# Optimization experiments

Hardware: AMD Instinct MI355X
Metric: run time of the kernel (lower is better)

Reference implementation:

```python
import jax, jax.numpy as jnp
import numpy as np

B, S, NX, NH = 2, 2048, 1024, 16
HD = NX // NH  # head dim = 64


def setup_inputs() -> dict:
    key = jax.random.key(0)
    k1, k2, k3 = jax.random.split(key, 3)
    x = jax.random.normal(k1, (B, S, NX), dtype=jnp.float32)
    w_attn = jax.random.normal(k2, (NX, 3 * NX), dtype=jnp.float32) * 0.02
    b_attn = jnp.zeros((3 * NX,), dtype=jnp.float32)
    w_proj = jax.random.normal(k3, (NX, NX), dtype=jnp.float32) * 0.02
    b_proj = jnp.zeros((NX,), dtype=jnp.float32)
    return {"x": x, "w_attn": w_attn, "b_attn": b_attn, "w_proj": w_proj, "b_proj": b_proj}


def _split_heads(t):
    # [B, S, NX] -> [B, NH, S, HD]
    b, s, _ = t.shape
    return t.reshape(b, s, NH, HD).transpose(0, 2, 1, 3)


def reference(x, w_attn, b_attn, w_proj, b_proj):
    # c_attn: Conv1D == affine projection to fused QKV
    qkv = jnp.einsum("bsi,io->bso", x, w_attn) + b_attn  # [B, S, 3*NX]
    q, k, v = jnp.split(qkv, 3, axis=2)
    q, k, v = _split_heads(q), _split_heads(k), _split_heads(v)  # [B, NH, S, HD]

    # scaled dot-product scores (scale=True)
    w = jnp.einsum("bhqd,bhkd->bhqk", q, k) / jnp.sqrt(jnp.asarray(HD, dtype=q.dtype))

    # causal mask via multiply-subtract (matches TF: w*b - 10000*(1-b))
    nd = ns = S
    i = jnp.arange(nd)[:, None]
    j = jnp.arange(ns)[None, :]
    b = (i >= j - ns + nd).astype(w.dtype)  # [nd, ns]
    w = w * b - 10000.0 * (1.0 - b)

    w = jax.nn.softmax(w, axis=-1)  # stable_softmax
    # attn_dropout / head_mask: identity (inference, no head mask)

    a = jnp.einsum("bhqk,bhkd->bhqd", w, v)  # [B, NH, S, HD]
    # merge heads -> [B, S, NX]
    a = a.transpose(0, 2, 1, 3).reshape(B, S, NX)
    # c_proj
    out = jnp.einsum("bsi,io->bso", a, w_proj) + b_proj
    return out
```

## Files before the change

kernel.cpp:

```cpp
#include <hip/hip_runtime.h>
#include <stdint.h>

typedef __attribute__((ext_vector_type(8))) short short8;
typedef __attribute__((ext_vector_type(4))) float f32x4;
typedef __attribute__((ext_vector_type(16))) float f32x16;
typedef __attribute__((ext_vector_type(4))) unsigned short ushort4v;
typedef __attribute__((ext_vector_type(2))) int int2v;

#define BB 2
#define SS 2048
#define NXDIM 1024
#define NHEADS 16
#define HDIM 64

__device__ __forceinline__ unsigned short f2bf(float f){
  unsigned int u = __float_as_uint(f);
  u += 0x7fffu + ((u >> 16) & 1u);
  return (unsigned short)(u >> 16);
}

__device__ __forceinline__ void gload_lds16(const void* g, void* l){
  __builtin_amdgcn_global_load_lds((const __attribute__((address_space(1))) void*)g,
                                   (__attribute__((address_space(3))) void*)l, 16, 0, 0);
}

__device__ __forceinline__ unsigned cvt_pk_bf16(float lo, float hi){
  unsigned r;
  asm("v_cvt_pk_bf16_f32 %0, %1, %2" : "=v"(r) : "v"(lo), "v"(hi));
  return r;
}

__device__ __forceinline__ int2v ds_tr_b16(unsigned addr){
  int2v r;
  asm volatile("ds_read_b64_tr_b16 %0, %1" : "=v"(r) : "v"(addr));
  return r;
}

__device__ __forceinline__ int2v plswap(int a, int b){
  return __builtin_amdgcn_permlane32_swap(a, b, false, false);
}
__device__ __forceinline__ float plmax(float x){
  int2v r = plswap(__float_as_int(x), __float_as_int(x));
  return fmaxf(__int_as_float(r.x), __int_as_float(r.y));
}
__device__ __forceinline__ float pladd(float x){
  int2v r = plswap(__float_as_int(x), __float_as_int(x));
  return __int_as_float(r.x) + __int_as_float(r.y);
}

__global__ __launch_bounds__(256) void f32_to_bf16_k(const float* __restrict__ in,
                                                     unsigned short* __restrict__ out, int n4){
  int i = blockIdx.x * 256 + threadIdx.x;
  if (i >= n4) return;
  float4 v = ((const float4*)in)[i];
  ushort4v r = { f2bf(v.x), f2bf(v.y), f2bf(v.z), f2bf(v.w) };
  ((ushort4v*)out)[i] = r;
}

__global__ __launch_bounds__(256) void transpose_bf16_k(const float* __restrict__ in,
                                                        unsigned short* __restrict__ out,
                                                        int R, int C){
  __shared__ float t[32][33];
  const int bx = blockIdx.x * 32, by = blockIdx.y * 32;
  const int tx = threadIdx.x, ty = threadIdx.y;
  #pragma unroll
  for (int i = ty; i < 32; i += 8)
    t[i][tx] = in[(size_t)(by + i) * C + bx + tx];
  __syncthreads();
  #pragma unroll
  for (int i = ty; i < 32; i += 8)
    out[(size_t)(bx + i) * R + by + tx] = f2bf(t[tx][i]);
}

__global__ __launch_bounds__(256) void gemm2_64_k(const unsigned short* __restrict__ A,
                                                  const unsigned short* __restrict__ BT,
                                                  const float* __restrict__ bias,
                                                  float* __restrict__ Cout,
                                                  int M, int N, int K)
{
  __shared__ unsigned short As[64*32];
  __shared__ unsigned short Bs[64*32];
  const int tid = threadIdx.x;
  const int w = tid >> 6, lane = tid & 63;
  const int l15 = lane & 15, g = lane >> 4;
  const int wr = w >> 1, wc = w & 1;
  const int m0 = blockIdx.y * 64, n0 = blockIdx.x * 64;

  f32x4 acc[2][2];
  #pragma unroll
  for (int m=0;m<2;m++)
    #pragma unroll
    for (int n=0;n<2;n++) acc[m][n] = (f32x4){0.f,0.f,0.f,0.f};

  const int srow_in = lane >> 2;
  const int scol = (lane & 3) * 8;

  for (int k0 = 0; k0 < K; k0 += 32){
    __syncthreads();
    gload_lds16(A  + (size_t)(m0 + w*16 + srow_in) * K + (k0 + scol), &As[(w*16)*32]);
    gload_lds16(BT + (size_t)(n0 + w*16 + srow_in) * K + (k0 + scol), &Bs[(w*16)*32]);
    __syncthreads();

    short8 af[2], bf[2];
    #pragma unroll
    for (int m=0;m<2;m++) af[m] = *(const short8*)&As[(wr*32 + m*16 + l15)*32 + g*8];
    #pragma unroll
    for (int n=0;n<2;n++) bf[n] = *(const short8*)&Bs[(wc*32 + n*16 + l15)*32 + g*8];
    #pragma unroll
    for (int m=0;m<2;m++)
      #pragma unroll
      for (int n=0;n<2;n++)
        acc[m][n] = __builtin_amdgcn_mfma_f32_16x16x32_bf16(af[m], bf[n], acc[m][n], 0, 0, 0);
  }

  const int crow0 = m0 + wr*32;
  const int ccol0 = n0 + wc*32;
  #pragma unroll
  for (int n=0;n<2;n++){
    const int col = ccol0 + n*16 + l15;
    const float bv = bias[col];
    #pragma unroll
    for (int m=0;m<2;m++){
      #pragma unroll
      for (int r=0;r<4;r++){
        const int row = crow0 + m*16 + g*4 + r;
        Cout[(size_t)row * N + col] = acc[m][n][r] + bv;
      }
    }
  }
}

__global__ __launch_bounds__(512) void gemm256_k(const unsigned short* __restrict__ A,
                                                 const unsigned short* __restrict__ BT,
                                                 const float* __restrict__ bias,
                                                 unsigned short* __restrict__ Cout,
                                                 int M, int N, int K)
{
  __shared__ unsigned short lds[57344];
  unsigned short* As0 = lds;
  unsigned short* Bs0 = lds + 32768;
  const int tid = threadIdx.x;
  const int w = tid >> 6, lane = tid & 63;
  const int l15 = lane & 15, g = lane >> 4;
  const int wm = w >> 2, wn = w & 3;
  const int m0 = blockIdx.y * 256, n0 = blockIdx.x * 192;

  f32x4 acc[8][3];
  #pragma unroll
  for (int m=0;m<8;m++)
    #pragma unroll
    for (int n=0;n<3;n++) acc[m][n] = (f32x4){0.f,0.f,0.f,0.f};

  const int srow = lane >> 3;
  const int scol = 8 * ((lane & 7) ^ (lane >> 3));

  auto stageA = [&](int bi, int k0, int j){
    const int r = w*32 + j*8 + srow;
    gload_lds16(A + (size_t)(m0 + r) * K + (k0 + scol), As0 + bi*16384 + (w*32 + j*8)*64);
  };
  auto stageB = [&](int bi, int k0, int j){
    const int r = w*24 + j*8 + srow;
    gload_lds16(BT + (size_t)(n0 + r) * K + (k0 + scol), Bs0 + bi*12288 + (w*24 + j*8)*64);
  };

  #pragma unroll
  for (int j=0;j<4;j++) stageA(0, 0, j);
  #pragma unroll
  for (int j=0;j<3;j++) stageB(0, 0, j);
  asm volatile("s_waitcnt vmcnt(0)" ::: "memory");
  __syncthreads();

  const int niter = K >> 6;
  int cur = 0;

  for (int t = 0; t < niter; ++t){
    const int k1 = (t+1) << 6;
    if (t+1 < niter){
      #pragma unroll
      for (int j=0;j<4;j++) stageA(cur^1, k1, j);
      #pragma unroll
      for (int j=0;j<3;j++) stageB(cur^1, k1, j);
    }

    const char* Ab = (const char*)(As0 + cur*16384);
    const char* Bb = (const char*)(Bs0 + cur*12288);

    short8 bf[3][2];
    #pragma unroll
    for (int nf=0;nf<3;nf++){
      const int row = wn*48 + nf*16 + l15;
      #pragma unroll
      for (int kk=0;kk<2;kk++)
        bf[nf][kk] = *(const short8*)(Bb + row*128 + ((kk*64 + g*16) ^ ((l15&7)<<4)));
    }

    #pragma unroll
    for (int ph=0; ph<4; ++ph){
      short8 af[2][2];
      #pragma unroll
      for (int i=0;i<2;i++){
        const int mf = ph*2 + i;
        const int row = wm*128 + mf*16 + l15;
        #pragma unroll
        for (int kk=0;kk<2;kk++)
          af[i][kk] = *(const short8*)(Ab + row*128 + ((kk*64 + g*16) ^ ((l15&7)<<4)));
      }
      asm volatile("s_waitcnt lgkmcnt(0)" ::: "memory");
      __builtin_amdgcn_sched_barrier(0);

      __builtin_amdgcn_s_setprio(1);
      #pragma unroll
      for (int i=0;i<2;i++)
        #pragma unroll
        for (int nf=0;nf<3;nf++)
          #pragma unroll
          for (int kk=0;kk<2;kk++)
            acc[ph*2+i][nf] = __builtin_amdgcn_mfma_f32_16x16x32_bf16(af[i][kk], bf[nf][kk],
                                                                      acc[ph*2+i][nf], 0, 0, 0);
      __builtin_amdgcn_s_setprio(0);
    }

    asm volatile("s_waitcnt vmcnt(0)" ::: "memory");
    __syncthreads();
    cur ^= 1;
  }

  unsigned short* ct = lds;
  #pragma unroll
  for (int nf=0;nf<3;nf++){
    const int col = wn*48 + nf*16 + l15;
    const float bv = bias[n0 + col];
    #pragma unroll
    for (int mf=0;mf<8;mf++){
      #pragma unroll
      for (int r=0;r<4;r++)
        ct[(wm*128 + mf*16 + g*4 + r)*192 + col] = f2bf(acc[mf][nf][r] + bv);
    }
  }
  __syncthreads();
  #pragma unroll
  for (int u = 0; u < 12; ++u){
    const int idx = u*512 + tid;
    const int row = idx / 24, sl = idx % 24;
    *(short8*)(Cout + (size_t)(m0 + row) * N + n0 + sl*8) = *(const short8*)&ct[row*192 + sl*8];
  }
}

__global__ __launch_bounds__(512) void attn_k(const unsigned short* __restrict__ qkv,
                                              unsigned short* __restrict__ aout)
{
  const int xy = ((int)blockIdx.x + (int)blockIdx.y) & 15;
  const int qb = blockIdx.z ? xy : (15 - xy);
  const int h = blockIdx.y, b = blockIdx.z;
  const int tid = threadIdx.x;
  const int w = tid >> 6, lane = tid & 63;
  const int l31 = lane & 31, hi = lane >> 5;
  const int qw = w >> 1, p = w & 1;

  __shared__ unsigned short lds[32768];
  unsigned short* Ksb = lds;
  unsigned short* Vsb = lds + 16384;

  const size_t rs = 3 * NXDIM;
  const unsigned short* Qg = qkv + (size_t)b * SS * rs + h * HDIM;
  const unsigned short* Kg = Qg + NXDIM;
  const unsigned short* Vg = Qg + 2 * NXDIM;

  const int q0w = qb*128 + qw*32;
  const int q   = q0w + l31;
  const int qw_hi = q0w + 31;

  short8 qf[4];
  #pragma unroll
  for (int c=0;c<4;c++)
    qf[c] = *(const short8*)(Qg + (size_t)q * rs + c*16 + 8*hi);

  f32x16 O0, O1;
  #pragma unroll
  for (int r=0;r<16;r++){ O0[r]=0.f; O1[r]=0.f; }
  float m_run = -1e30f, l_run = 0.f;
  const float SC2 = 0.125f * 1.44269504089f;
  const float THRR = 44.36f;

  const int krow_in = lane >> 3;
  const int kcol    = 8 * ((lane & 7) ^ (lane >> 3));
  const int v_d     = ((lane >> 3) & 3) * 16 + 8 * (lane & 1);
  const unsigned vtr_base = (unsigned)(size_t)Vsb + 8u*(unsigned)lane + 768u*(unsigned)hi;

  auto stage = [&](int bi, int tt){
    unsigned short* Kd = Ksb + (p*2 + bi)*4096;
    unsigned short* Vd = Vsb + (p*2 + bi)*4096;
    #pragma unroll
    for (int j=0;j<2;j++){
      const int ch = qw*2 + j;
      const int krow = tt*64 + ch*8 + krow_in;
      gload_lds16(Kg + (size_t)krow * rs + kcol, Kd + ch*512);
      const int vkv = tt*64 + (ch*2 + hi)*4 + ((lane>>1)&3);
      gload_lds16(Vg + (size_t)vkv * rs + v_d, Vd + ch*512);
    }
  };

  const int tmax = 2*qb + 1;
  stage(0, p);
  __syncthreads();
  int cur = 0;

  for (int t = p; t <= tmax; t += 2){
    if (t + 2 <= tmax) stage(cur^1, t+2);

    const char* Kb = (const char*)(Ksb + (p*2 + cur)*4096);
    const unsigned vb = vtr_base + (unsigned)((p*2 + cur)*8192);

    #pragma unroll
    for (int kvs=0;kvs<2;kvs++){
      const int kv_lo = t*64 + kvs*32;
      if (kv_lo > qw_hi) continue;

      f32x16 S;
      #pragma unroll
      for (int r=0;r<16;r++) S[r] = 0.f;
      __builtin_amdgcn_s_setprio(1);
      #pragma unroll
      for (int c=0;c<4;c++){
        const int row = kvs*32 + l31;
        short8 kf = *(const short8*)(Kb + row*128 + ((c*32 + 16*hi) ^ ((row&7)<<4)));
        S = __builtin_amdgcn_mfma_f32_32x32x16_bf16(kf, qf[c], S, 0, 0, 0);
      }
      __builtin_amdgcn_s_setprio(0);

      int2v tv[8];
      #pragma unroll
      for (int c=0;c<2;c++)
        #pragma unroll
        for (int dh=0;dh<2;dh++)
          #pragma unroll
          for (int eb=0;eb<2;eb++)
            tv[c*4+dh*2+eb] = ds_tr_b16(vb + (unsigned)((kvs*8 + c*4 + eb)*512 + dh*256));

      float mA=-1e30f, mB=-1e30f, mC=-1e30f, mD=-1e30f;
      if (kv_lo + 31 > q0w){
        #pragma unroll
        for (int r=0;r<16;r+=4){
          const int kvb = kv_lo + 8*(r>>2) + 4*hi;
          float s0 = (kvb+0 <= q) ? S[r+0] : -1e30f;
          float s1 = (kvb+1 <= q) ? S[r+1] : -1e30f;
          float s2 = (kvb+2 <= q) ? S[r+2] : -1e30f;
          float s3 = (kvb+3 <= q) ? S[r+3] : -1e30f;
          S[r+0]=s0; S[r+1]=s1; S[r+2]=s2; S[r+3]=s3;
          mA = fmaxf(mA, s0); mB = fmaxf(mB, s1); mC = fmaxf(mC, s2); mD = fmaxf(mD, s3);
        }
      } else {
        #pragma unroll
        for (int r=0;r<16;r+=4){
          mA = fmaxf(mA, S[r+0]); mB = fmaxf(mB, S[r+1]);
          mC = fmaxf(mC, S[r+2]); mD = fmaxf(mD, S[r+3]);
        }
      }
      float mx = fmaxf(fmaxf(mA,mB), fmaxf(mC,mD));
      mx = plmax(mx);

      if (!__all(mx <= m_run + THRR)){
        const float m_new = fmaxf(m_run, mx);
        const float corr = __builtin_exp2f((m_run - m_new) * SC2);
        m_run = m_new;
        l_run *= corr;
        #pragma unroll
        for (int r=0;r<16;r++){ O0[r] *= corr; O1[r] *= corr; }
      }
      const float msc = m_run * SC2;

      float lA=0.f, lB=0.f, lC=0.f, lD=0.f;
      #pragma unroll
      for (int r=0;r<16;r+=4){
        float p0=__builtin_exp2f(__builtin_fmaf(S[r+0],SC2,-msc));
        float p1=__builtin_exp2f(__builtin_fmaf(S[r+1],SC2,-msc));
        float p2=__builtin_exp2f(__builtin_fmaf(S[r+2],SC2,-msc));
        float p3=__builtin_exp2f(__builtin_fmaf(S[r+3],SC2,-msc));
        S[r+0]=p0; S[r+1]=p1; S[r+2]=p2; S[r+3]=p3;
        lA+=p0; lB+=p1; lC+=p2; lD+=p3;
      }
      float ls = (lA+lB) + (lC+lD);
      ls = pladd(ls);
      l_run += ls;

      unsigned pk[8];
      #pragma unroll
      for (int i=0;i<8;i++) pk[i] = cvt_pk_bf16(S[2*i], S[2*i+1]);
      short8 pfrag[2];
      #pragma unroll
      for (int c=0;c<2;c++){
        int2v r0 = plswap((int)pk[4*c+0], (int)pk[4*c+2]);
        int2v r1 = plswap((int)pk[4*c+1], (int)pk[4*c+3]);
        union { unsigned u[4]; short8 s; } pw;
        pw.u[0] = (unsigned)r0.x; pw.u[1] = (unsigned)r1.x;
        pw.u[2] = (unsigned)r0.y; pw.u[3] = (unsigned)r1.y;
        pfrag[c] = pw.s;
      }

      asm volatile("s_waitcnt lgkmcnt(0)" ::: "memory");
      __builtin_amdgcn_sched_barrier(0);

      __builtin_amdgcn_s_setprio(1);
      #pragma unroll
      for (int c=0;c<2;c++){
        union { int2v t[2]; short8 s; } v0, v1;
        v0.t[0] = tv[c*4+0]; v0.t[1] = tv[c*4+1];
        v1.t[0] = tv[c*4+2]; v1.t[1] = tv[c*4+3];
        O0 = __builtin_amdgcn_mfma_f32_32x32x16_bf16(v0.s, pfrag[c], O0, 0, 0, 0);
        O1 = __builtin_amdgcn_mfma_f32_32x32x16_bf16(v1.s, pfrag[c], O1, 0, 0, 0);
      }
      __builtin_amdgcn_s_setprio(0);
    }

    __syncthreads();
    cur ^= 1;
  }

  float* sm = (float*)lds + qw * (64*34);
  if (p){
    #pragma unroll
    for (int r=0;r<16;r++){ sm[lane*34 + r] = O0[r]; sm[lane*34 + 16 + r] = O1[r]; }
    sm[lane*34 + 32] = m_run;
    sm[lane*34 + 33] = l_run;
  }
  __syncthreads();
  if (!p){
    const float m1 = sm[lane*34 + 32], l1 = sm[lane*34 + 33];
    const float mm = fmaxf(m_run, m1);
    const float c0 = __builtin_exp2f((m_run - mm) * SC2);
    const float c1 = __builtin_exp2f((m1 - mm) * SC2);
    const float inv = 1.f / (l_run*c0 + l1*c1);
    unsigned short* dst = aout + ((size_t)b*SS + q) * NXDIM + h*HDIM;
    #pragma unroll
    for (int g4=0; g4<4; g4++){
      ushort4v a0, a1;
      #pragma unroll
      for (int i=0;i<4;i++){
        a0[i] = f2bf((O0[4*g4+i]*c0 + sm[lane*34 + 4*g4+i]*c1) * inv);
        a1[i] = f2bf((O1[4*g4+i]*c0 + sm[lane*34 + 16 + 4*g4+i]*c1) * inv);
      }
      *(ushort4v*)(dst + 8*g4 + 4*hi)      = a0;
      *(ushort4v*)(dst + 32 + 8*g4 + 4*hi) = a1;
    }
  }
}

extern "C" void kernel_launch(void* const* d_in, const int* in_sizes, int n_in,
                              void* d_out, int out_size, void* d_ws, size_t ws_size,
                              hipStream_t stream){
  (void)in_sizes; (void)n_in; (void)out_size; (void)ws_size;
  const float* x      = (const float*)d_in[0];
  const float* w_attn = (const float*)d_in[1];
  const float* b_attn = (const float*)d_in[2];
  const float* w_proj = (const float*)d_in[3];
  const float* b_proj = (const float*)d_in[4];
  float* out = (float*)d_out;

  unsigned short* xb   = (unsigned short*)d_ws;
  unsigned short* waT  = xb  + (size_t)4096*1024;
  unsigned short* wpT  = waT + (size_t)3072*1024;
  unsigned short* qkv  = wpT + (size_t)1024*1024;
  unsigned short* aout = qkv + (size_t)4096*3072;

  f32_to_bf16_k<<<4096, 256, 0, stream>>>(x, xb, 4096*1024/4);
  transpose_bf16_k<<<dim3(3072/32, 1024/32), dim3(32,8), 0, stream>>>(w_attn, waT, 1024, 3072);
  transpose_bf16_k<<<dim3(1024/32, 1024/32), dim3(32,8), 0, stream>>>(w_proj, wpT, 1024, 1024);

  gemm256_k<<<dim3(3072/192, 4096/256), 512, 0, stream>>>(xb, waT, b_attn, qkv, 4096, 3072, 1024);
  attn_k<<<dim3(SS/128, NHEADS, BB), 512, 0, stream>>>(qkv, aout);
  gemm2_64_k<<<dim3(1024/64, 4096/64), 256, 0, stream>>>(aout, wpT, b_proj, out, 4096, 1024, 1024);
}
```

Before: 113.4 us.

## Shrink attention blocks to 64 queries and merge both weight transposes into one launch

The attention kernel now uses 256-thread blocks covering 64 query rows each, launching twice as many blocks with half the LDS. The KV double-buffered prefetch is replaced by single-buffer staging with a sync before and after each tile, so two wave pairs split KV tiles by parity. The two weight-transpose kernels are fused into a single launch that picks its matrix from the block index. This aims for more blocks in flight and better causal load balance, plus one fewer launch, at the cost of losing overlap between global loads and compute.

Measured after the change: 144.9 us. 1.28x slower.

```diff
diff --git a/kernel.cpp b/kernel.cpp
--- a/kernel.cpp
+++ b/kernel.cpp
@@ -57,12 +57,19 @@
   ((ushort4v*)out)[i] = r;
 }
 
-__global__ __launch_bounds__(256) void transpose_bf16_k(const float* __restrict__ in,
-                                                        unsigned short* __restrict__ out,
-                                                        int R, int C){
+__global__ __launch_bounds__(256) void transpose2_k(const float* __restrict__ wa,
+                                                    unsigned short* __restrict__ waT,
+                                                    const float* __restrict__ wp,
+                                                    unsigned short* __restrict__ wpT){
   __shared__ float t[32][33];
-  const int bx = blockIdx.x * 32, by = blockIdx.y * 32;
-  const int tx = threadIdx.x, ty = threadIdx.y;
+  const bool second = blockIdx.x >= 96;
+  const float* in = second ? wp : wa;
+  unsigned short* out = second ? wpT : waT;
+  const int C = second ? 1024 : 3072;
+  const int R = 1024;
+  const int bx = (second ? ((int)blockIdx.x - 96) : (int)blockIdx.x) * 32;
+  const int by = blockIdx.y * 32;
+  const int tx = threadIdx.x & 31, ty = threadIdx.x >> 5;
   #pragma unroll
   for (int i = ty; i < 32; i += 8)
     t[i][tx] = in[(size_t)(by + i) * C + bx + tx];
@@ -246,27 +253,27 @@
   }
 }
 
-__global__ __launch_bounds__(512) void attn_k(const unsigned short* __restrict__ qkv,
+__global__ __launch_bounds__(256) void attn_k(const unsigned short* __restrict__ qkv,
                                               unsigned short* __restrict__ aout)
 {
-  const int xy = ((int)blockIdx.x + (int)blockIdx.y) & 15;
-  const int qb = blockIdx.z ? xy : (15 - xy);
+  const int xy = ((int)blockIdx.x + (int)blockIdx.y) & 31;
+  const int qb = blockIdx.z ? xy : (31 - xy);
   const int h = blockIdx.y, b = blockIdx.z;
   const int tid = threadIdx.x;
   const int w = tid >> 6, lane = tid & 63;
   const int l31 = lane & 31, hi = lane >> 5;
   const int qw = w >> 1, p = w & 1;
 
-  __shared__ unsigned short lds[32768];
+  __shared__ unsigned short lds[16384];
   unsigned short* Ksb = lds;
-  unsigned short* Vsb = lds + 16384;
+  unsigned short* Vsb = lds + 8192;
 
   const size_t rs = 3 * NXDIM;
   const unsigned short* Qg = qkv + (size_t)b * SS * rs + h * HDIM;
   const unsigned short* Kg = Qg + NXDIM;
   const unsigned short* Vg = Qg + 2 * NXDIM;
 
-  const int q0w = qb*128 + qw*32;
+  const int q0w = qb*64 + qw*32;
   const int q   = q0w + l31;
   const int qw_hi = q0w + 31;
 
@@ -285,14 +292,15 @@
   const int krow_in = lane >> 3;
   const int kcol    = 8 * ((lane & 7) ^ (lane >> 3));
   const int v_d     = ((lane >> 3) & 3) * 16 + 8 * (lane & 1);
-  const unsigned vtr_base = (unsigned)(size_t)Vsb + 8u*(unsigned)lane + 768u*(unsigned)hi;
-
-  auto stage = [&](int bi, int tt){
-    unsigned short* Kd = Ksb + (p*2 + bi)*4096;
-    unsigned short* Vd = Vsb + (p*2 + bi)*4096;
-    #pragma unroll
-    for (int j=0;j<2;j++){
-      const int ch = qw*2 + j;
+  const unsigned vtr_base = (unsigned)(size_t)Vsb + (unsigned)(p*8192)
+                          + 8u*(unsigned)lane + 768u*(unsigned)hi;
+
+  auto stage = [&](int tt){
+    unsigned short* Kd = Ksb + p*4096;
+    unsigned short* Vd = Vsb + p*4096;
+    #pragma unroll
+    for (int j=0;j<4;j++){
+      const int ch = qw*4 + j;
       const int krow = tt*64 + ch*8 + krow_in;
       gload_lds16(Kg + (size_t)krow * rs + kcol, Kd + ch*512);
       const int vkv = tt*64 + (ch*2 + hi)*4 + ((lane>>1)&3);
@@ -300,123 +308,122 @@
     }
   };
 
-  const int tmax = 2*qb + 1;
-  stage(0, p);
-  __syncthreads();
-  int cur = 0;
-
-  for (int t = p; t <= tmax; t += 2){
-    if (t + 2 <= tmax) stage(cur^1, t+2);
-
-    const char* Kb = (const char*)(Ksb + (p*2 + cur)*4096);
-    const unsigned vb = vtr_base + (unsigned)((p*2 + cur)*8192);
-
-    #pragma unroll
-    for (int kvs=0;kvs<2;kvs++){
-      const int kv_lo = t*64 + kvs*32;
-      if (kv_lo > qw_hi) continue;
-
-      f32x16 S;
-      #pragma unroll
-      for (int r=0;r<16;r++) S[r] = 0.f;
-      __builtin_amdgcn_s_setprio(1);
-      #pragma unroll
-      for (int c=0;c<4;c++){
-        const int row = kvs*32 + l31;
-        short8 kf = *(const short8*)(Kb + row*128 + ((c*32 + 16*hi) ^ ((row&7)<<4)));
-        S = __builtin_amdgcn_mfma_f32_32x32x16_bf16(kf, qf[c], S, 0, 0, 0);
+  for (int i = 0; 2*i <= qb; ++i){
+    const int t = 2*i + p;
+    const bool act = (t <= qb);
+    if (act) stage(t);
+    __syncthreads();
+
+    if (act){
+      const char* Kb = (const char*)(Ksb + p*4096);
+      const unsigned vb = vtr_base;
+
+      #pragma unroll
+      for (int kvs=0;kvs<2;kvs++){
+        const int kv_lo = t*64 + kvs*32;
+        if (kv_lo > qw_hi) continue;
+
+        f32x16 S;
+        #pragma unroll
+        for (int r=0;r<16;r++) S[r] = 0.f;
+        __builtin_amdgcn_s_setprio(1);
+        #pragma unroll
+        for (int c=0;c<4;c++){
+          const int row = kvs*32 + l31;
+          short8 kf = *(const short8*)(Kb + row*128 + ((c*32 + 16*hi) ^ ((row&7)<<4)));
+          S = __builtin_amdgcn_mfma_f32_32x32x16_bf16(kf, qf[c], S, 0, 0, 0);
+        }
+        __builtin_amdgcn_s_setprio(0);
+
+        int2v tv[8];
+        #pragma unroll
+        for (int c=0;c<2;c++)
+          #pragma unroll
+          for (int dh=0;dh<2;dh++)
+            #pragma unroll
+            for (int eb=0;eb<2;eb++)
+              tv[c*4+dh*2+eb] = ds_tr_b16(vb + (unsigned)((kvs*8 + c*4 + eb)*512 + dh*256));
+
+        float mA=-1e30f, mB=-1e30f, mC=-1e30f, mD=-1e30f;
+        if (kv_lo + 31 > q0w){
+          #pragma unroll
+          for (int r=0;r<16;r+=4){
+            const int kvb = kv_lo + 8*(r>>2) + 4*hi;
+            float s0 = (kvb+0 <= q) ? S[r+0] : -1e30f;
+            float s1 = (kvb+1 <= q) ? S[r+1] : -1e30f;
+            float s2 = (kvb+2 <= q) ? S[r+2] : -1e30f;
+            float s3 = (kvb+3 <= q) ? S[r+3] : -1e30f;
+            S[r+0]=s0; S[r+1]=s1; S[r+2]=s2; S[r+3]=s3;
+            mA = fmaxf(mA, s0); mB = fmaxf(mB, s1); mC = fmaxf(mC, s2); mD = fmaxf(mD, s3);
+          }
+        } else {
+          #pragma unroll
+          for (int r=0;r<16;r+=4){
+            mA = fmaxf(mA, S[r+0]); mB = fmaxf(mB, S[r+1]);
+            mC = fmaxf(mC, S[r+2]); mD = fmaxf(mD, S[r+3]);
+          }
+        }
+        float mx = fmaxf(fmaxf(mA,mB), fmaxf(mC,mD));
+        mx = plmax(mx);
+
+        if (!__all(mx <= m_run + THRR)){
+          const float m_new = fmaxf(m_run, mx);
+          const float corr = __builtin_exp2f((m_run - m_new) * SC2);
+          m_run = m_new;
+          l_run *= corr;
+          #pragma unroll
+          for (int r=0;r<16;r++){ O0[r] *= corr; O1[r] *= corr; }
+        }
+        const float msc = m_run * SC2;
+
+        float lA=0.f, lB=0.f, lC=0.f, lD=0.f;
+        #pragma unroll
+        for (int r=0;r<16;r+=4){
+          float p0=__builtin_exp2f(__builtin_fmaf(S[r+0],SC2,-msc));
+          float p1=__builtin_exp2f(__builtin_fmaf(S[r+1],SC2,-msc));
+          float p2=__builtin_exp2f(__builtin_fmaf(S[r+2],SC2,-msc));
+          float p3=__builtin_exp2f(__builtin_fmaf(S[r+3],SC2,-msc));
+          S[r+0]=p0; S[r+1]=p1; S[r+2]=p2; S[r+3]=p3;
+          lA+=p0; lB+=p1; lC+=p2; lD+=p3;
+        }
+        float ls = (lA+lB) + (lC+lD);
+        ls = pladd(ls);
+        l_run += ls;
+
+        unsigned pk[8];
+        #pragma unroll
+        for (int i2=0;i2<8;i2++) pk[i2] = cvt_pk_bf16(S[2*i2], S[2*i2+1]);
+        short8 pfrag[2];
+        #pragma unroll
+        for (int c=0;c<2;c++){
+          int2v r0 = plswap((int)pk[4*c+0], (int)pk[4*c+2]);
+          int2v r1 = plswap((int)pk[4*c+1], (int)pk[4*c+3]);
+          union { unsigned u[4]; short8 s; } pw;
+          pw.u[0] = (unsigned)r0.x; pw.u[1] = (unsigned)r1.x;
+          pw.u[2] = (unsigned)r0.y; pw.u[3] = (unsigned)r1.y;
+          pfrag[c] = pw.s;
+        }
+
+        asm volatile("s_waitcnt lgkmcnt(0)" ::: "memory");
+        __builtin_amdgcn_sched_barrier(0);
+
+        __builtin_amdgcn_s_setprio(1);
+        #pragma unroll
+        for (int c=0;c<2;c++){
+          union { int2v t[2]; short8 s; } v0, v1;
+          v0.t[0] = tv[c*4+0]; v0.t[1] = tv[c*4+1];
+          v1.t[0] = tv[c*4+2]; v1.t[1] = tv[c*4+3];
+          O0 = __builtin_amdgcn_mfma_f32_32x32x16_bf16(v0.s, pfrag[c], O0, 0, 0, 0);
+          O1 = __builtin_amdgcn_mfma_f32_32x32x16_bf16(v1.s, pfrag[c], O1, 0, 0, 0);
+        }
+        __builtin_amdgcn_s_setprio(0);
       }
-      __builtin_amdgcn_s_setprio(0);
-
-      int2v tv[8];
-      #pragma unroll
-      for (int c=0;c<2;c++)
-        #pragma unroll
-        for (int dh=0;dh<2;dh++)
-          #pragma unroll
-          for (int eb=0;eb<2;eb++)
-            tv[c*4+dh*2+eb] = ds_tr_b16(vb + (unsigned)((kvs*8 + c*4 + eb)*512 + dh*256));
-
-      float mA=-1e30f, mB=-1e30f, mC=-1e30f, mD=-1e30f;
-      if (kv_lo + 31 > q0w){
-        #pragma unroll
-        for (int r=0;r<16;r+=4){
-          const int kvb = kv_lo + 8*(r>>2) + 4*hi;
-          float s0 = (kvb+0 <= q) ? S[r+0] : -1e30f;
-          float s1 = (kvb+1 <= q) ? S[r+1] : -1e30f;
-          float s2 = (kvb+2 <= q) ? S[r+2] : -1e30f;
-          float s3 = (kvb+3 <= q) ? S[r+3] : -1e30f;
-          S[r+0]=s0; S[r+1]=s1; S[r+2]=s2; S[r+3]=s3;
-          mA = fmaxf(mA, s0); mB = fmaxf(mB, s1); mC = fmaxf(mC, s2); mD = fmaxf(mD, s3);
-        }
-      } else {
-        #pragma unroll
-        for (int r=0;r<16;r+=4){
-          mA = fmaxf(mA, S[r+0]); mB = fmaxf(mB, S[r+1]);
-          mC = fmaxf(mC, S[r+2]); mD = fmaxf(mD, S[r+3]);
-        }
-      }
-      float mx = fmaxf(fmaxf(mA,mB), fmaxf(mC,mD));
-      mx = plmax(mx);
-
-      if (!__all(mx <= m_run + THRR)){
-        const float m_new = fmaxf(m_run, mx);
-        const float corr = __builtin_exp2f((m_run - m_new) * SC2);
-        m_run = m_new;
-        l_run *= corr;
-        #pragma unroll
-        for (int r=0;r<16;r++){ O0[r] *= corr; O1[r] *= corr; }
-      }
-      const float msc = m_run * SC2;
-
-      float lA=0.f, lB=0.f, lC=0.f, lD=0.f;
-      #pragma unroll
-      for (int r=0;r<16;r+=4){
-        float p0=__builtin_exp2f(__builtin_fmaf(S[r+0],SC2,-msc));
-        float p1=__builtin_exp2f(__builtin_fmaf(S[r+1],SC2,-msc));
-        float p2=__builtin_exp2f(__builtin_fmaf(S[r+2],SC2,-msc));
-        float p3=__builtin_exp2f(__builtin_fmaf(S[r+3],SC2,-msc));
-        S[r+0]=p0; S[r+1]=p1; S[r+2]=p2; S[r+3]=p3;
-        lA+=p0; lB+=p1; lC+=p2; lD+=p3;
-      }
-      float ls = (lA+lB) + (lC+lD);
-      ls = pladd(ls);
-      l_run += ls;
-
-      unsigned pk[8];
-      #pragma unroll
-      for (int i=0;i<8;i++) pk[i] = cvt_pk_bf16(S[2*i], S[2*i+1]);
-      short8 pfrag[2];
-      #pragma unroll
-      for (int c=0;c<2;c++){
-        int2v r0 = plswap((int)pk[4*c+0], (int)pk[4*c+2]);
-        int2v r1 = plswap((int)pk[4*c+1], (int)pk[4*c+3]);
-        union { unsigned u[4]; short8 s; } pw;
-        pw.u[0] = (unsigned)r0.x; pw.u[1] = (unsigned)r1.x;
-        pw.u[2] = (unsigned)r0.y; pw.u[3] = (unsigned)r1.y;
-        pfrag[c] = pw.s;
-      }
-
-      asm volatile("s_waitcnt lgkmcnt(0)" ::: "memory");
-      __builtin_amdgcn_sched_barrier(0);
-
-      __builtin_amdgcn_s_setprio(1);
-      #pragma unroll
-      for (int c=0;c<2;c++){
-        union { int2v t[2]; short8 s; } v0, v1;
-        v0.t[0] = tv[c*4+0]; v0.t[1] = tv[c*4+1];
-        v1.t[0] = tv[c*4+2]; v1.t[1] = tv[c*4+3];
-        O0 = __builtin_amdgcn_mfma_f32_32x32x16_bf16(v0.s, pfrag[c], O0, 0, 0, 0);
-        O1 = __builtin_amdgcn_mfma_f32_32x32x16_bf16(v1.s, pfrag[c], O1, 0, 0, 0);
-      }
-      __builtin_amdgcn_s_setprio(0);
     }
 
     __syncthreads();
-    cur ^= 1;
-  }
-
-  float* sm = (float*)lds + qw * (64*34);
+  }
+
+  float* sm = (float*)lds + qw * 2176;
   if (p){
     #pragma unroll
     for (int r=0;r<16;r++){ sm[lane*34 + r] = O0[r]; sm[lane*34 + 16 + r] = O1[r]; }
@@ -435,9 +442,9 @@
     for (int g4=0; g4<4; g4++){
       ushort4v a0, a1;
       #pragma unroll
-      for (int i=0;i<4;i++){
-        a0[i] = f2bf((O0[4*g4+i]*c0 + sm[lane*34 + 4*g4+i]*c1) * inv);
-        a1[i] = f2bf((O1[4*g4+i]*c0 + sm[lane*34 + 16 + 4*g4+i]*c1) * inv);
+      for (int i2=0;i2<4;i2++){
+        a0[i2] = f2bf((O0[4*g4+i2]*c0 + sm[lane*34 + 4*g4+i2]*c1) * inv);
+        a1[i2] = f2bf((O1[4*g4+i2]*c0 + sm[lane*34 + 16 + 4*g4+i2]*c1) * inv);
       }
       *(ushort4v*)(dst + 8*g4 + 4*hi)      = a0;
       *(ushort4v*)(dst + 32 + 8*g4 + 4*hi) = a1;
@@ -463,10 +470,9 @@
   unsigned short* aout = qkv + (size_t)4096*3072;
 
   f32_to_bf16_k<<<4096, 256, 0, stream>>>(x, xb, 4096*1024/4);
-  transpose_bf16_k<<<dim3(3072/32, 1024/32), dim3(32,8), 0, stream>>>(w_attn, waT, 1024, 3072);
-  transpose_bf16_k<<<dim3(1024/32, 1024/32), dim3(32,8), 0, stream>>>(w_proj, wpT, 1024, 1024);
+  transpose2_k<<<dim3(128, 32), 256, 0, stream>>>(w_attn, waT, w_proj, wpT);
 
   gemm256_k<<<dim3(3072/192, 4096/256), 512, 0, stream>>>(xb, waT, b_attn, qkv, 4096, 3072, 1024);
-  attn_k<<<dim3(SS/128, NHEADS, BB), 512, 0, stream>>>(qkv, aout);
+  attn_k<<<dim3(SS/64, NHEADS, BB), 256, 0, stream>>>(qkv, aout);
   gemm2_64_k<<<dim3(1024/64, 4096/64), 256, 0, stream>>>(aout, wpT, b_proj, out, 4096, 1024, 1024);
 }
```
